# Optimization experiments

Measured on AMD Instinct MI355X. Metric: run time of the kernel, lower is better.

The kernel has to match this reference:

```python
import jax, jax.numpy as jnp
import numpy as np

N_NODES = 50000
N_EDGES = 800000
D_FEAT = 128
HIDDEN = 128
OUT = 128


def setup_inputs() -> dict:
    key = jax.random.key(0)
    ks = jax.random.split(key, 8)
    sc_in = 1.0 / np.sqrt(D_FEAT)
    sc_h = 1.0 / np.sqrt(HIDDEN)
    return {
        "x": jax.random.normal(ks[0], (N_NODES, D_FEAT), dtype=jnp.float32),
        "edge_index": jax.random.randint(ks[1], (2, N_EDGES), 0, N_NODES, dtype=jnp.int64),
        "W1_l": jax.random.normal(ks[2], (D_FEAT, HIDDEN), dtype=jnp.float32) * sc_in,
        "b1_l": jnp.zeros((HIDDEN,), dtype=jnp.float32),
        "W1_r": jax.random.normal(ks[3], (D_FEAT, HIDDEN), dtype=jnp.float32) * sc_in,
        "W2_l": jax.random.normal(ks[4], (HIDDEN, OUT), dtype=jnp.float32) * sc_h,
        "b2_l": jnp.zeros((OUT,), dtype=jnp.float32),
        "W2_r": jax.random.normal(ks[5], (HIDDEN, OUT), dtype=jnp.float32) * sc_h,
    }


def _sage_conv(x, src, dst, W_l, b_l, W_r, n_nodes):
    # mean aggregation of source features onto destination nodes
    msgs = x[src]  # [E, d] irregular gather
    summed = jax.ops.segment_sum(msgs, dst, num_segments=n_nodes)
    cnt = jax.ops.segment_sum(jnp.ones((src.shape[0],), x.dtype), dst, num_segments=n_nodes)
    aggr = summed / jnp.maximum(cnt, 1.0)[:, None]  # empty neighborhoods -> 0
    # PyG SAGEConv: lin_l(aggr) + lin_r(x_root); bias lives on lin_l
    return aggr @ W_l + b_l + x @ W_r


def reference(x, edge_index, W1_l, b1_l, W1_r, W2_l, b2_l, W2_r):
    src, dst = edge_index[0], edge_index[1]
    n = x.shape[0]
    h = _sage_conv(x, src, dst, W1_l, b1_l, W1_r, n)
    h = jax.nn.relu(h)
    out = _sage_conv(h, src, dst, W2_l, b2_l, W2_r, n)
    return out
```

## Files before the change

### kernel.cpp

```cpp
#include <hip/hip_runtime.h>

#define NN 50000
#define NE 800000
#define D 128
#define SEGBITS 8
#define SEGSZ 256
#define NSEG 196
#define GRID_A 1024
#define EPB ((NE + GRID_A - 1) / GRID_A)
#define FLAT (NSEG * GRID_A)
#define SBLK ((FLAT + 255) / 256)

typedef __attribute__((ext_vector_type(8))) short short8;
typedef __attribute__((ext_vector_type(4))) float f32x4;

__device__ inline unsigned short f2bf(float f) {
    unsigned u = __builtin_bit_cast(unsigned, f);
    unsigned r = (u + 0x7fffu + ((u >> 16) & 1u)) >> 16;
    return (unsigned short)r;
}
__device__ inline float bflo(unsigned u) { return __builtin_bit_cast(float, u << 16); }
__device__ inline float bfhi(unsigned u) { return __builtin_bit_cast(float, u & 0xffff0000u); }


__global__ __launch_bounds__(256) void histA_kernel(const int* __restrict__ dst,
        int* __restrict__ bh,
        const float* __restrict__ W0, const float* __restrict__ W1,
        const float* __restrict__ W2, const float* __restrict__ W3,
        unsigned short* __restrict__ wf) {
    __shared__ int h[NSEG];
    int t = threadIdx.x;
    int b = blockIdx.x;
    if (t < NSEG) h[t] = 0;
    __syncthreads();
    int beg = b * EPB;
    int end = min(beg + EPB, NE);
    for (int e = beg + t; e < end; e += 256) atomicAdd(&h[dst[e] >> SEGBITS], 1);
    __syncthreads();
    if (t < NSEG) bh[t * GRID_A + b] = h[t];
    if (b < 32) {
        int tg = b * 256 + t;
        int w = tg >> 11, rem = tg & 2047;
        int f = rem >> 6, l = rem & 63;
        int ct = f >> 2, kk = f & 3;
        int col = ct * 16 + (l & 15);
        int k0 = kk * 32 + (l >> 4) * 8;
        const float* W = (w == 0) ? W0 : (w == 1) ? W1 : (w == 2) ? W2 : W3;
        unsigned short* o = wf + (size_t)w * 16384 + ((size_t)f * 64 + l) * 8;
        #pragma unroll
        for (int e = 0; e < 8; ++e) o[e] = f2bf(W[(k0 + e) * D + col]);
    }
}

__global__ __launch_bounds__(256) void partialS_kernel(const int* __restrict__ bh,
        int* __restrict__ bsum) {
    __shared__ int s[256];
    int t = threadIdx.x;
    int i = blockIdx.x * 256 + t;
    s[t] = (i < FLAT) ? bh[i] : 0;
    __syncthreads();
    #pragma unroll
    for (int off = 128; off > 0; off >>= 1) {
        if (t < off) s[t] += s[t + off];
        __syncthreads();
    }
    if (t == 0) bsum[blockIdx.x] = s[0];
}

__global__ __launch_bounds__(1024) void scanS_kernel(const int* __restrict__ bsum,
        int* __restrict__ boff) {
    __shared__ int s[1024];
    int t = threadIdx.x;
    int v = (t < SBLK) ? bsum[t] : 0;
    s[t] = v;
    __syncthreads();
    #pragma unroll
    for (int off = 1; off < 1024; off <<= 1) {
        int u = (t >= off) ? s[t - off] : 0;
        __syncthreads();
        s[t] += u;
        __syncthreads();
    }
    if (t < SBLK) boff[t] = s[t] - v;
}

__global__ __launch_bounds__(256) void scan2S_kernel(const int* __restrict__ bh,
        const int* __restrict__ boff, int* __restrict__ bases,
        int* __restrict__ segBase) {
    __shared__ int s[256];
    int t = threadIdx.x;
    int i = blockIdx.x * 256 + t;
    int v = (i < FLAT) ? bh[i] : 0;
    s[t] = v;
    __syncthreads();
    #pragma unroll
    for (int off = 1; off < 256; off <<= 1) {
        int u = (t >= off) ? s[t - off] : 0;
        __syncthreads();
        s[t] += u;
        __syncthreads();
    }
    if (i < FLAT) {
        int excl = s[t] - v + boff[blockIdx.x];
        bases[i] = excl;
        if ((i & (GRID_A - 1)) == 0) segBase[i >> 10] = excl;
    }
    if (i == 0) segBase[NSEG] = NE;
}

__global__ __launch_bounds__(256) void scatA_kernel(const int* __restrict__ src,
        const int* __restrict__ dst, const int* __restrict__ bases,
        unsigned* __restrict__ bucket) {
    __shared__ int cur[NSEG];
    int t = threadIdx.x;
    if (t < NSEG) cur[t] = bases[t * GRID_A + blockIdx.x];
    __syncthreads();
    int beg = blockIdx.x * EPB;
    int end = min(beg + EPB, NE);
    for (int e = beg + t; e < end; e += 256) {
        int d = dst[e];
        int sg = d >> SEGBITS;
        int p = atomicAdd(&cur[sg], 1);
        bucket[p] = ((unsigned)(d & (SEGSZ - 1)) << 24) | (unsigned)src[e];
    }
}

__global__ __launch_bounds__(256) void buildB_kernel(const unsigned* __restrict__ bucket,
        const int* __restrict__ segBase, int* __restrict__ rowptr, int* __restrict__ csr) {
    __shared__ int h[SEGSZ];
    __shared__ int s[SEGSZ];
    int sg = blockIdx.x;
    int t = threadIdx.x;
    int beg = segBase[sg], end = segBase[sg + 1];
    h[t] = 0;
    __syncthreads();
    for (int i = beg + t; i < end; i += 256) atomicAdd(&h[bucket[i] >> 24], 1);
    __syncthreads();
    int v = h[t];
    s[t] = v;
    __syncthreads();
    #pragma unroll
    for (int off = 1; off < 256; off <<= 1) {
        int u = (t >= off) ? s[t - off] : 0;
        __syncthreads();
        s[t] += u;
        __syncthreads();
    }
    int excl = beg + s[t] - v;
    int n = sg * SEGSZ + t;
    if (n <= NN) rowptr[n] = excl;
    h[t] = excl;
    __syncthreads();
    for (int i = beg + t; i < end; i += 256) {
        unsigned u = bucket[i];
        int p = atomicAdd(&h[u >> 24], 1);
        csr[p] = (int)(u & 0xFFFFFFu);
    }
}


template<int AFP32>
__global__ __launch_bounds__(256, 1) void gemm_kernel(const void* __restrict__ Av,
        const unsigned short* __restrict__ WfL, const unsigned short* __restrict__ WfR,
        unsigned short* __restrict__ Yb, unsigned short* __restrict__ Zb, int nrows) {
    __shared__ short8 sW[4096];

    for (int i = threadIdx.x; i < 2048; i += 256) {
        sW[i]        = ((const short8*)WfL)[i];
        sW[i + 2048] = ((const short8*)WfR)[i];
    }
    __syncthreads();

    int wv = threadIdx.x >> 6, l = threadIdx.x & 63;
    int r15 = l & 15, kg = l >> 4;
    int row0 = blockIdx.x * 128 + wv * 32;

    short8 a[2][4];
    #pragma unroll
    for (int rt = 0; rt < 2; ++rt) {
        #pragma unroll
        for (int kk = 0; kk < 4; ++kk) {
            int row = row0 + rt * 16 + r15;
            row = min(row, nrows - 1);
            int off = kk * 32 + kg * 8;
            if (AFP32) {
                const float* A = (const float*)Av;
                float4 p = *(const float4*)(A + (size_t)row * D + off);
                float4 q = *(const float4*)(A + (size_t)row * D + off + 4);
                short8 v;
                v[0] = (short)f2bf(p.x); v[1] = (short)f2bf(p.y);
                v[2] = (short)f2bf(p.z); v[3] = (short)f2bf(p.w);
                v[4] = (short)f2bf(q.x); v[5] = (short)f2bf(q.y);
                v[6] = (short)f2bf(q.z); v[7] = (short)f2bf(q.w);
                a[rt][kk] = v;
            } else {
                const unsigned short* A = (const unsigned short*)Av;
                a[rt][kk] = *(const short8*)(A + (size_t)row * D + off);
            }
        }
    }

    f32x4 accY[2][8] = {};
    f32x4 accZ[2][8] = {};
    #pragma unroll
    for (int ct = 0; ct < 8; ++ct) {
        #pragma unroll
        for (int kk = 0; kk < 4; ++kk) {
            short8 bL = sW[(ct * 4 + kk) * 64 + l];
            short8 bR = sW[2048 + (ct * 4 + kk) * 64 + l];
            accY[0][ct] = __builtin_amdgcn_mfma_f32_16x16x32_bf16(a[0][kk], bL, accY[0][ct], 0, 0, 0);
            accY[1][ct] = __builtin_amdgcn_mfma_f32_16x16x32_bf16(a[1][kk], bL, accY[1][ct], 0, 0, 0);
            accZ[0][ct] = __builtin_amdgcn_mfma_f32_16x16x32_bf16(a[0][kk], bR, accZ[0][ct], 0, 0, 0);
            accZ[1][ct] = __builtin_amdgcn_mfma_f32_16x16x32_bf16(a[1][kk], bR, accZ[1][ct], 0, 0, 0);
        }
    }

    #pragma unroll
    for (int rt = 0; rt < 2; ++rt) {
        #pragma unroll
        for (int ct = 0; ct < 8; ++ct) {
            #pragma unroll
            for (int i = 0; i < 4; ++i) {
                int row = row0 + rt * 16 + kg * 4 + i;
                if (row < nrows) {
                    int col = ct * 16 + r15;
                    Yb[(size_t)row * D + col] = f2bf(accY[rt][ct][i]);
                    Zb[(size_t)row * D + col] = f2bf(accZ[rt][ct][i]);
                }
            }
        }
    }
}


template<int RELU, int OUTBF16>
__global__ __launch_bounds__(256) void agg_ep_kernel(const unsigned short* __restrict__ Yb,
        const unsigned short* __restrict__ Zb, const float* __restrict__ bias,
        const int* __restrict__ rowptr, const int* __restrict__ csr,
        void* __restrict__ outp) {
    int lane = threadIdx.x & 63;
    int sub = lane >> 4;
    int m = lane & 15;
    int wv = (blockIdx.x << 2) + (threadIdx.x >> 6);
    int nw = gridDim.x << 2;
    float bb[8];
    #pragma unroll
    for (int e = 0; e < 8; ++e) bb[e] = bias[m * 8 + e];

    for (int node = wv; node < NN; node += nw) {
        int beg = rowptr[node], end = rowptr[node + 1];
        float acc[8] = {};
        int j = beg + sub;
        for (; j + 4 < end; j += 8) {
            int sa = csr[j];
            int sb = csr[j + 4];
            uint4 ua = *(const uint4*)(Yb + (size_t)sa * D + m * 8);
            uint4 ub = *(const uint4*)(Yb + (size_t)sb * D + m * 8);
            acc[0] += bflo(ua.x); acc[1] += bfhi(ua.x);
            acc[2] += bflo(ua.y); acc[3] += bfhi(ua.y);
            acc[4] += bflo(ua.z); acc[5] += bfhi(ua.z);
            acc[6] += bflo(ua.w); acc[7] += bfhi(ua.w);
            acc[0] += bflo(ub.x); acc[1] += bfhi(ub.x);
            acc[2] += bflo(ub.y); acc[3] += bfhi(ub.y);
            acc[4] += bflo(ub.z); acc[5] += bfhi(ub.z);
            acc[6] += bflo(ub.w); acc[7] += bfhi(ub.w);
        }
        if (j < end) {
            int sa = csr[j];
            uint4 ua = *(const uint4*)(Yb + (size_t)sa * D + m * 8);
            acc[0] += bflo(ua.x); acc[1] += bfhi(ua.x);
            acc[2] += bflo(ua.y); acc[3] += bfhi(ua.y);
            acc[4] += bflo(ua.z); acc[5] += bfhi(ua.z);
            acc[6] += bflo(ua.w); acc[7] += bfhi(ua.w);
        }
        #pragma unroll
        for (int e = 0; e < 8; ++e) {
            acc[e] += __shfl_xor(acc[e], 16, 64);
            acc[e] += __shfl_xor(acc[e], 32, 64);
        }
        if (sub == 0) {
            float inv = (end > beg) ? 1.f / (float)(end - beg) : 0.f;
            uint4 uz = *(const uint4*)(Zb + (size_t)node * D + m * 8);
            float v[8];
            v[0] = acc[0] * inv + bb[0] + bflo(uz.x);
            v[1] = acc[1] * inv + bb[1] + bfhi(uz.x);
            v[2] = acc[2] * inv + bb[2] + bflo(uz.y);
            v[3] = acc[3] * inv + bb[3] + bfhi(uz.y);
            v[4] = acc[4] * inv + bb[4] + bflo(uz.z);
            v[5] = acc[5] * inv + bb[5] + bfhi(uz.z);
            v[6] = acc[6] * inv + bb[6] + bflo(uz.w);
            v[7] = acc[7] * inv + bb[7] + bfhi(uz.w);
            if (RELU) {
                #pragma unroll
                for (int e = 0; e < 8; ++e) v[e] = fmaxf(v[e], 0.f);
            }
            if (OUTBF16) {
                uint4 o;
                o.x = (unsigned)f2bf(v[0]) | ((unsigned)f2bf(v[1]) << 16);
                o.y = (unsigned)f2bf(v[2]) | ((unsigned)f2bf(v[3]) << 16);
                o.z = (unsigned)f2bf(v[4]) | ((unsigned)f2bf(v[5]) << 16);
                o.w = (unsigned)f2bf(v[6]) | ((unsigned)f2bf(v[7]) << 16);
                *(uint4*)((unsigned short*)outp + (size_t)node * D + m * 8) = o;
            } else {
                float* op = (float*)outp + (size_t)node * D + m * 8;
                f32x4 o1 = {v[0], v[1], v[2], v[3]};
                f32x4 o2 = {v[4], v[5], v[6], v[7]};
                __builtin_nontemporal_store(o1, (f32x4*)op);
                __builtin_nontemporal_store(o2, (f32x4*)(op + 4));
            }
        }
    }
}


extern "C" void kernel_launch(void* const* d_in, const int* in_sizes, int n_in,
                              void* d_out, int out_size, void* d_ws, size_t ws_size,
                              hipStream_t stream) {
    const float* x   = (const float*)d_in[0];
    const int*   ei  = (const int*)d_in[1];
    const float* W1l = (const float*)d_in[2];
    const float* b1  = (const float*)d_in[3];
    const float* W1r = (const float*)d_in[4];
    const float* W2l = (const float*)d_in[5];
    const float* b2  = (const float*)d_in[6];
    const float* W2r = (const float*)d_in[7];
    float* out = (float*)d_out;

    const int N = NN, E = NE;
    const int* src = ei;
    const int* dst = ei + E;

    char* ws = (char*)d_ws;
    size_t off = 0;
    auto alloc = [&](size_t bytes) -> void* {
        void* p = ws + off;
        off += (bytes + 255) & ~(size_t)255;
        return p;
    };
    int* rowptr  = (int*)alloc((size_t)(N + 1) * 4);
    int* csr     = (int*)alloc((size_t)E * 4);
    int* bh      = (int*)alloc((size_t)FLAT * 4);
    int* bases   = (int*)alloc((size_t)FLAT * 4);
    int* bsumS   = (int*)alloc((size_t)SBLK * 4);
    int* boffS   = (int*)alloc((size_t)SBLK * 4);
    int* segBase = (int*)alloc((size_t)(NSEG + 1) * 4);
    unsigned* bucket = (unsigned*)alloc((size_t)E * 4);
    unsigned short* hb  = (unsigned short*)alloc((size_t)N * D * 2);
    unsigned short* Yb  = (unsigned short*)alloc((size_t)N * D * 2);
    unsigned short* Zb  = (unsigned short*)alloc((size_t)N * D * 2);
    unsigned short* wf  = (unsigned short*)alloc((size_t)4 * 16384 * 2);

    histA_kernel<<<GRID_A, 256, 0, stream>>>(dst, bh, W1l, W1r, W2l, W2r, wf);
    partialS_kernel<<<SBLK, 256, 0, stream>>>(bh, bsumS);
    scanS_kernel<<<1, 1024, 0, stream>>>(bsumS, boffS);
    scan2S_kernel<<<SBLK, 256, 0, stream>>>(bh, boffS, bases, segBase);
    scatA_kernel<<<GRID_A, 256, 0, stream>>>(src, dst, bases, bucket);
    buildB_kernel<<<NSEG, 256, 0, stream>>>(bucket, segBase, rowptr, csr);

    unsigned short* wf1l = wf;
    unsigned short* wf1r = wf + 16384;
    unsigned short* wf2l = wf + 2 * 16384;
    unsigned short* wf2r = wf + 3 * 16384;

    int gblocks = (N + 127) / 128;

    gemm_kernel<1><<<gblocks, 256, 0, stream>>>(x, wf1l, wf1r, Yb, Zb, N);
    agg_ep_kernel<1, 1><<<2048, 256, 0, stream>>>(Yb, Zb, b1, rowptr, csr, hb);

    gemm_kernel<0><<<gblocks, 256, 0, stream>>>(hb, wf2l, wf2r, Yb, Zb, N);
    agg_ep_kernel<0, 0><<<2048, 256, 0, stream>>>(Yb, Zb, b2, rowptr, csr, out);
}
```

Before: 132.6 us.

## Drop LDS weight staging and split GEMM into sequential Y and Z passes

```diff
diff --git a/kernel.cpp b/kernel.cpp
--- a/kernel.cpp
+++ b/kernel.cpp
@@ -160,17 +160,9 @@
 
 
 template<int AFP32>
-__global__ __launch_bounds__(256, 1) void gemm_kernel(const void* __restrict__ Av,
+__global__ __launch_bounds__(256) void gemm_kernel(const void* __restrict__ Av,
         const unsigned short* __restrict__ WfL, const unsigned short* __restrict__ WfR,
         unsigned short* __restrict__ Yb, unsigned short* __restrict__ Zb, int nrows) {
-    __shared__ short8 sW[4096];
-
-    for (int i = threadIdx.x; i < 2048; i += 256) {
-        sW[i]        = ((const short8*)WfL)[i];
-        sW[i + 2048] = ((const short8*)WfR)[i];
-    }
-    __syncthreads();
-
     int wv = threadIdx.x >> 6, l = threadIdx.x & 63;
     int r15 = l & 15, kg = l >> 4;
     int row0 = blockIdx.x * 128 + wv * 32;
@@ -200,32 +192,51 @@
         }
     }
 
-    f32x4 accY[2][8] = {};
-    f32x4 accZ[2][8] = {};
-    #pragma unroll
-    for (int ct = 0; ct < 8; ++ct) {
-        #pragma unroll
-        for (int kk = 0; kk < 4; ++kk) {
-            short8 bL = sW[(ct * 4 + kk) * 64 + l];
-            short8 bR = sW[2048 + (ct * 4 + kk) * 64 + l];
-            accY[0][ct] = __builtin_amdgcn_mfma_f32_16x16x32_bf16(a[0][kk], bL, accY[0][ct], 0, 0, 0);
-            accY[1][ct] = __builtin_amdgcn_mfma_f32_16x16x32_bf16(a[1][kk], bL, accY[1][ct], 0, 0, 0);
-            accZ[0][ct] = __builtin_amdgcn_mfma_f32_16x16x32_bf16(a[0][kk], bR, accZ[0][ct], 0, 0, 0);
-            accZ[1][ct] = __builtin_amdgcn_mfma_f32_16x16x32_bf16(a[1][kk], bR, accZ[1][ct], 0, 0, 0);
-        }
-    }
-
-    #pragma unroll
-    for (int rt = 0; rt < 2; ++rt) {
+    const short8* BL = (const short8*)WfL;
+    const short8* BR = (const short8*)WfR;
+
+    {
+        f32x4 acc[2][8] = {};
         #pragma unroll
         for (int ct = 0; ct < 8; ++ct) {
             #pragma unroll
-            for (int i = 0; i < 4; ++i) {
-                int row = row0 + rt * 16 + kg * 4 + i;
-                if (row < nrows) {
-                    int col = ct * 16 + r15;
-                    Yb[(size_t)row * D + col] = f2bf(accY[rt][ct][i]);
-                    Zb[(size_t)row * D + col] = f2bf(accZ[rt][ct][i]);
+            for (int kk = 0; kk < 4; ++kk) {
+                short8 bf = BL[(ct * 4 + kk) * 64 + l];
+                acc[0][ct] = __builtin_amdgcn_mfma_f32_16x16x32_bf16(a[0][kk], bf, acc[0][ct], 0, 0, 0);
+                acc[1][ct] = __builtin_amdgcn_mfma_f32_16x16x32_bf16(a[1][kk], bf, acc[1][ct], 0, 0, 0);
+            }
+        }
+        #pragma unroll
+        for (int rt = 0; rt < 2; ++rt) {
+            #pragma unroll
+            for (int ct = 0; ct < 8; ++ct) {
+                #pragma unroll
+                for (int i = 0; i < 4; ++i) {
+                    int row = row0 + rt * 16 + kg * 4 + i;
+                    if (row < nrows) Yb[(size_t)row * D + ct * 16 + r15] = f2bf(acc[rt][ct][i]);
+                }
+            }
+        }
+    }
+    {
+        f32x4 acc[2][8] = {};
+        #pragma unroll
+        for (int ct = 0; ct < 8; ++ct) {
+            #pragma unroll
+            for (int kk = 0; kk < 4; ++kk) {
+                short8 bf = BR[(ct * 4 + kk) * 64 + l];
+                acc[0][ct] = __builtin_amdgcn_mfma_f32_16x16x32_bf16(a[0][kk], bf, acc[0][ct], 0, 0, 0);
+                acc[1][ct] = __builtin_amdgcn_mfma_f32_16x16x32_bf16(a[1][kk], bf, acc[1][ct], 0, 0, 0);
+            }
+        }
+        #pragma unroll
+        for (int rt = 0; rt < 2; ++rt) {
+            #pragma unroll
+            for (int ct = 0; ct < 8; ++ct) {
+                #pragma unroll
+                for (int i = 0; i < 4; ++i) {
+                    int row = row0 + rt * 16 + kg * 4 + i;
+                    if (row < nrows) Zb[(size_t)row * D + ct * 16 + r15] = f2bf(acc[rt][ct][i]);
                 }
             }
         }
```

New measurement: 138.6 us. 4.6% more time.
